# Performance work log

Hardware: AMD Instinct MI355X
Metric: run time of the kernel (lower is better)

Reference implementation:

```python
import jax, jax.numpy as jnp
import numpy as np

NQ, NT, BSZ, E, NH = 100, 197, 128, 768, 12
HD = E // NH
EPS = 1e-12  # torch F.normalize default eps


def _l2norm(x, axis=-1):
    n = jnp.linalg.norm(x, axis=axis, keepdims=True)
    return x / jnp.maximum(n, EPS)


def setup_inputs() -> dict:
    rng = jax.random.key(0)
    ks = jax.random.split(rng, 10)
    s = 0.02  # xavier-ish scale for weights
    return {
        "query": jax.random.normal(ks[0], (NQ, BSZ, E), jnp.float32),
        "key": jax.random.normal(ks[1], (NT, BSZ, E), jnp.float32),
        "value": jax.random.normal(ks[2], (NT, BSZ, E), jnp.float32),
        "in_proj_weight": jax.random.normal(ks[3], (3 * E, E), jnp.float32) * s,
        "in_proj_bias": jnp.zeros((3 * E,), jnp.float32),
        "out_proj_weight": jax.random.normal(ks[4], (E, E), jnp.float32) * s,
        "out_proj_bias": jnp.zeros((E,), jnp.float32),
        "temperature": jnp.ones((NH, 1, 1), jnp.float32),
        "q_mapper": jax.random.normal(ks[5], (1, NT, NQ), jnp.float32),
        "x_mapper": jax.random.normal(ks[6], (1, NQ, NT), jnp.float32),
    }


def reference(query, key, value, in_proj_weight, in_proj_bias,
              out_proj_weight, out_proj_bias, temperature, q_mapper, x_mapper):
    nq, bsz, e = query.shape
    nt = key.shape[0]
    # packed in-projection: split into q/k/v weights
    wq, wk, wv = jnp.split(in_proj_weight, 3, axis=0)
    bq, bk, bv = jnp.split(in_proj_bias, 3, axis=0)
    q = query @ wq.T + bq   # [Nq, bsz, E]
    k = key @ wk.T + bk     # [Nt, bsz, E]
    v = value @ wv.T + bv   # [Nt, bsz, E]
    # reshape to [bsz, nh, hd, N] (channel-major for cross-covariance attn)
    q = q.reshape(nq, bsz, NH, HD).transpose(1, 2, 3, 0)  # [b, h, d, Nq]
    k = k.reshape(nt, bsz, NH, HD).transpose(1, 2, 3, 0)  # [b, h, d, Nt]
    v = v.reshape(nt, bsz, NH, HD).transpose(1, 2, 3, 0)  # [b, h, d, Nt]
    # normalize channel vectors over tokens
    qn = _l2norm(q)
    kn = _l2norm(k)
    # mappers: normalize over last dim, then shape to [Nq, Nt] operators
    qm_op = _l2norm(q_mapper[0])  # [Nt, Nq] normalized over Nq; transpose below
    xm_op = _l2norm(x_mapper[0])  # [Nq, Nt] normalized over Nt
    # qm = q @ q_mapper^T : [b,h,d,Nq] x [Nq,Nt] -> [b,h,d,Nt]
    qm = jnp.einsum('bhdq,tq->bhdt', qn, qm_op)
    # cross-covariance attention over channels: [b,h,d,d]
    attn = jnp.einsum('bhdt,bhet->bhde', qm, kn) * temperature[None]  # temp [nh,1,1] broadcasts per-head
    attn = jax.nn.softmax(attn, axis=-1)
    x = jnp.einsum('bhde,bhet->bhdt', attn, v)        # [b,h,d,Nt]
    out = jnp.einsum('bhdt,qt->bhdq', x, xm_op)       # [b,h,d,Nq]
    # back to [Nq, bsz, E]
    out = out.transpose(3, 0, 1, 2).reshape(nq, bsz, e)
    out = out @ out_proj_weight.T + out_proj_bias
    return out
```

## Files before the change

kernel.cpp:

```cpp
#include <hip/hip_runtime.h>
#include <hip/hip_bf16.h>

using bf16 = __hip_bfloat16;

constexpr int NQ  = 100;
constexpr int NT  = 197;
constexpr int BSZ = 128;
constexpr int EMB = 768;
constexpr int NHD = 12;
constexpr int HDD = 64;
constexpr int COLS = BSZ * EMB;
constexpr int M_Q  = NQ * BSZ;
constexpr int M_KV = NT * BSZ;
constexpr int TPAD = 224;

constexpr size_t OFF_QP   = 256;
constexpr size_t SZ_QP    = (size_t)M_Q  * EMB * 4;
constexpr size_t OFF_A    = OFF_QP + SZ_QP;
constexpr size_t SZ_A     = (size_t)M_KV * EMB * 4;
constexpr size_t OFF_QINV = OFF_A + SZ_A;
constexpr size_t OFF_KINV = OFF_QINV + (size_t)COLS * 4;
constexpr size_t OFF_QMN  = OFF_KINV + (size_t)COLS * 4;
constexpr size_t OFF_XMN  = OFF_QMN + (size_t)NT * 128 * 4;
constexpr size_t OFF_G    = OFF_XMN + (size_t)NT * 128 * 4;
constexpr size_t OFF_W    = OFF_G + (size_t)COLS * 128 * 4;
constexpr size_t OFF_ZB   = OFF_QMN + 57344;
constexpr size_t OFF_G2   = OFF_G + (size_t)COLS * 128 * 2;
constexpr size_t OFF_WI16 = OFF_W + (size_t)COLS * TPAD * 2;
constexpr size_t OFF_QNT  = OFF_A + 20971520;
constexpr size_t OFF_WO16 = OFF_A + 46137344;

__device__ __forceinline__ float dl(const float* p) { return *p; }
__device__ __forceinline__ float dl(const bf16* p) { return __bfloat162float(*p); }

__device__ __forceinline__ ushort f2bf(float x) {
    union { float f; unsigned u; } v; v.f = x;
    unsigned r = v.u + 0x7FFFu + ((v.u >> 16) & 1u);
    return (ushort)(r >> 16);
}
__device__ __forceinline__ float bf2f(ushort x) {
    union { unsigned u; float f; } v; v.u = (unsigned)x << 16;
    return v.f;
}
__device__ __forceinline__ void dstore(float* p, float v) { *p = v; }
__device__ __forceinline__ void dstore(bf16* p, float v) { *p = __float2bfloat16(v); }

typedef __attribute__((ext_vector_type(8))) short short8;
typedef __attribute__((ext_vector_type(4))) short shortv4;
typedef __attribute__((ext_vector_type(4))) float f32x4;

__device__ __forceinline__ void gload16(const bf16* g, ushort* l) {
    __builtin_amdgcn_global_load_lds(
        (const __attribute__((address_space(1))) unsigned int*)g,
        (__attribute__((address_space(3))) unsigned int*)l, 16, 0, 0);
}

__device__ __forceinline__ int2 xcd_swz(int bx, int by, int gx, int gy) {
    const int nwg = gx * gy;
    const int L = by * gx + bx;
    const int q = nwg >> 3, r = nwg & 7;
    const int c = L & 7, i = L >> 3;
    const int wg = (c < r ? c * (q + 1) : r * (q + 1) + (c - r) * q) + i;
    return make_int2(wg % gx, wg / gx);
}

__global__ void k_zero(float* p, int n) {
    int i = blockIdx.x * 256 + threadIdx.x;
    if (i < n) p[i] = 0.f;
}

__global__ __launch_bounds__(256) void k_cvt(const float* __restrict__ src,
        bf16* __restrict__ dst, int n) {
    int i = (blockIdx.x * 256 + threadIdx.x) * 8;
    if (i >= n) return;
    float4 a = *(const float4*)(src + i), b = *(const float4*)(src + i + 4);
    short8 r;
    r[0] = (short)f2bf(a.x); r[1] = (short)f2bf(a.y); r[2] = (short)f2bf(a.z); r[3] = (short)f2bf(a.w);
    r[4] = (short)f2bf(b.x); r[5] = (short)f2bf(b.y); r[6] = (short)f2bf(b.z); r[7] = (short)f2bf(b.w);
    *(short8*)(dst + i) = r;
}

template <typename T>
__global__ __launch_bounds__(128) void k_qmn(const T* qm, bf16* dstT) {
    __shared__ float red[128];
    int t = blockIdx.x, q = threadIdx.x;
    float v = (q < NQ) ? dl(&qm[t * NQ + q]) : 0.f;
    red[q] = v * v;
    __syncthreads();
    for (int s = 64; s > 0; s >>= 1) { if (q < s) red[q] += red[q + s]; __syncthreads(); }
    float inv = 1.f / fmaxf(sqrtf(red[0]), 1e-12f);
    if (q < NQ) dstore(&dstT[(size_t)q * TPAD + t], v * inv);
}

template <typename T>
__global__ __launch_bounds__(256) void k_xmn(const T* xm, bf16* dstT) {
    __shared__ float red[256];
    int q = blockIdx.x, t = threadIdx.x;
    float v = (t < NT) ? dl(&xm[q * NT + t]) : 0.f;
    red[t] = v * v;
    __syncthreads();
    for (int s = 128; s > 0; s >>= 1) { if (t < s) red[t] += red[t + s]; __syncthreads(); }
    float inv = 1.f / fmaxf(sqrtf(red[0]), 1e-12f);
    if (t < NT) dstore(&dstT[(size_t)q * TPAD + t], v * inv);
}

template <int NR, int TP, int NORM>
__global__ __launch_bounds__(256) void k_trn(const bf16* __restrict__ src,
        bf16* __restrict__ dst) {
    __shared__ ushort tile[TP * 73];
    __shared__ float ssp[4][64];
    __shared__ float inv_s[64];
    const int col0 = blockIdx.x * 64;
    const int tid = threadIdx.x;
    const int c = tid & 63, tb = tid >> 6;
    float ss = 0.f;
#pragma unroll
    for (int it = 0; it < TP / 4; ++it) {
        int t = tb + it * 4;
        ushort v = 0;
        if (t < NR) v = *(const ushort*)&src[(size_t)t * COLS + col0 + c];
        tile[t * 73 + c] = v;
        if (NORM) { float f = bf2f(v); ss = fmaf(f, f, ss); }
    }
    if (NORM) {
        ssp[tb][c] = ss;
        __syncthreads();
        if (tid < 64) {
            float s = ssp[0][tid] + ssp[1][tid] + ssp[2][tid] + ssp[3][tid];
            inv_s[tid] = 1.f / fmaxf(sqrtf(s), 1e-12f);
        }
    }
    __syncthreads();
    constexpr int UPC = TP / 8;
#pragma unroll
    for (int it = 0; it < (64 * UPC) / 256; ++it) {
        int u = tid + it * 256;
        int cc = u / UPC, t0 = (u % UPC) * 8;
        float inv = NORM ? inv_s[cc] : 1.f;
        short8 s;
#pragma unroll
        for (int r = 0; r < 8; ++r) {
            ushort raw = tile[(t0 + r) * 73 + cc];
            s[r] = NORM ? (short)f2bf(bf2f(raw) * inv) : (short)raw;
        }
        *(short8*)&dst[(size_t)(col0 + cc) * TP + t0] = s;
    }
}

template <typename TC, typename TBias, bool CT = false>
__global__ __launch_bounds__(256) void k_gemm_mfma(
        const bf16* __restrict__ Ab, const bf16* __restrict__ Wb,
        TC* __restrict__ C, const TBias* __restrict__ bias,
        int M, int N, int K, int ldc) {
    __shared__ __align__(16) ushort As[128 * 32];
    __shared__ __align__(16) ushort Bs[128 * 32];
    const int t = threadIdx.x;
    const int2 bxy = xcd_swz(blockIdx.x, blockIdx.y, gridDim.x, gridDim.y);
    const int n0 = bxy.x * 128, m0 = bxy.y * 128;
    const int ln = t & 63, wv = t >> 6;
    const int ln15 = ln & 15, q8 = ln >> 4;
    const int mw = (wv & 1) * 64, nw = (wv >> 1) * 64;

    const int sr = ln >> 2, sk = (ln & 3) * 8;
    const bf16* gA = Ab + (size_t)(m0 + wv * 32 + sr) * K + sk;
    const bf16* gB = Wb + (size_t)(n0 + wv * 32 + sr) * K + sk;
    const size_t r16 = (size_t)16 * K;
    ushort* lA = &As[wv * 1024];
    ushort* lB = &Bs[wv * 1024];

    f32x4 acc[4][4] = {};
    for (int k0 = 0; k0 < K; k0 += 32) {
        gload16(gA + k0,       lA);
        gload16(gA + r16 + k0, lA + 512);
        gload16(gB + k0,       lB);
        gload16(gB + r16 + k0, lB + 512);
        __syncthreads();
        short8 a[4], b[4];
#pragma unroll
        for (int i = 0; i < 4; ++i)
            a[i] = *(const short8*)&As[(mw + i * 16 + ln15) * 32 + q8 * 8];
#pragma unroll
        for (int j = 0; j < 4; ++j)
            b[j] = *(const short8*)&Bs[(nw + j * 16 + ln15) * 32 + q8 * 8];
#pragma unroll
        for (int i = 0; i < 4; ++i)
#pragma unroll
            for (int j = 0; j < 4; ++j)
                acc[i][j] = __builtin_amdgcn_mfma_f32_16x16x32_bf16(a[i], b[j], acc[i][j], 0, 0, 0);
        __syncthreads();
    }
#pragma unroll
    for (int j = 0; j < 4; ++j) {
        const int n = n0 + nw + j * 16 + ln15;
        const float bv = dl(&bias[n]);
#pragma unroll
        for (int i = 0; i < 4; ++i) {
            const int mb = m0 + mw + i * 16 + q8 * 4;
            if constexpr (CT) {
                shortv4 s;
#pragma unroll
                for (int r = 0; r < 4; ++r) s[r] = (short)f2bf(acc[i][j][r] + bv);
                *(shortv4*)&C[(size_t)n * ldc + mb] = s;
            } else {
#pragma unroll
                for (int r = 0; r < 4; ++r)
                    dstore(&C[(size_t)(mb + r) * ldc + n], acc[i][j][r] + bv);
            }
        }
    }
}

template <typename T>
__global__ __launch_bounds__(256) void k_attn(
        const bf16* __restrict__ qnT, const bf16* __restrict__ g16,
        const bf16* __restrict__ w16T, const T* __restrict__ temp,
        bf16* __restrict__ xo) {
    const int h = blockIdx.x, b = blockIdx.y;
    const int tid = threadIdx.x;
    const int ln = tid & 63, wv = tid >> 6;
    const int ln15 = ln & 15, q8 = ln >> 4;
    const int colbase = b * EMB + h * HDD;
    __shared__ __align__(16) ushort smem[16384];
    char* sm = (char*)smem;

#pragma unroll
    for (int it = 0; it < 4; ++it) {
        int u = tid + it * 256;
        int e = u >> 4, q0 = (u & 15) * 8;
        short8 s = *(const short8*)&g16[(size_t)(colbase + e) * 128 + q0];
        *(short8*)(sm + ((e * 256 + q0 * 2) ^ ((e & 7) << 4))) = s;
    }
#pragma unroll
    for (int it = 0; it < 4; ++it) {
        int u = tid + it * 256;
        int d = u >> 4, q0 = (u & 15) * 8;
        short8 s = *(const short8*)&qnT[(size_t)(colbase + d) * 128 + q0];
        *(short8*)(sm + 16384 + ((d * 256 + q0 * 2) ^ ((d & 7) << 4))) = s;
    }
    __syncthreads();

    const int drow = 16 * wv + ln15;
    f32x4 acc[4] = {};
#pragma unroll
    for (int ks = 0; ks < 4; ++ks) {
        short8 bfrag = *(const short8*)(sm + 16384 +
            ((drow * 256 + ks * 64 + q8 * 16) ^ ((drow & 7) << 4)));
#pragma unroll
        for (int i = 0; i < 4; ++i) {
            int erow = i * 16 + ln15;
            short8 afrag = *(const short8*)(sm +
                ((erow * 256 + ks * 64 + q8 * 16) ^ ((erow & 7) << 4)));
            acc[i] = __builtin_amdgcn_mfma_f32_16x16x32_bf16(afrag, bfrag, acc[i], 0, 0, 0);
        }
    }

    const float tv = dl(&temp[h]);
    float p[4][4];
    float mx = -1e30f;
#pragma unroll
    for (int i = 0; i < 4; ++i)
#pragma unroll
        for (int r = 0; r < 4; ++r) { p[i][r] = acc[i][r] * tv; mx = fmaxf(mx, p[i][r]); }
    mx = fmaxf(mx, __shfl_xor(mx, 16, 64));
    mx = fmaxf(mx, __shfl_xor(mx, 32, 64));
    float sum = 0.f;
#pragma unroll
    for (int i = 0; i < 4; ++i)
#pragma unroll
        for (int r = 0; r < 4; ++r) { p[i][r] = __expf(p[i][r] - mx); sum += p[i][r]; }
    sum += __shfl_xor(sum, 16, 64);
    sum += __shfl_xor(sum, 32, 64);
    const float rs = 1.f / sum;

    __syncthreads();

#pragma unroll
    for (int i = 0; i < 4; ++i) {
        shortv4 s4;
#pragma unroll
        for (int r = 0; r < 4; ++r) s4[r] = (short)f2bf(p[i][r] * rs);
        *(shortv4*)(sm + 16384 + drow * 144 + q8 * 8 + 32 * i) = s4;
    }
#pragma unroll
    for (int it = 0; it < 4; ++it) {
        int u = tid + it * 256;
        int q = u >> 3, e0 = (u & 7) * 8;
        short8 s = *(const short8*)&w16T[(size_t)q * COLS + colbase + e0];
        *(short8*)(sm + ((q * 128 + e0 * 2) ^ ((q & 7) << 4))) = s;
    }
    __syncthreads();

    f32x4 o[7] = {};
#pragma unroll
    for (int ks = 0; ks < 2; ++ks) {
        short8 afrag = *(const short8*)(sm + 16384 + drow * 144 + ks * 64 + q8 * 16);
#pragma unroll
        for (int j = 0; j < 7; ++j) {
            int qrow = j * 16 + ln15;
            short8 bfrag = *(const short8*)(sm +
                ((qrow * 128 + ks * 64 + q8 * 16) ^ ((qrow & 7) << 4)));
            o[j] = __builtin_amdgcn_mfma_f32_16x16x32_bf16(afrag, bfrag, o[j], 0, 0, 0);
        }
    }
    const int dbase = h * HDD + 16 * wv + q8 * 4;
#pragma unroll
    for (int j = 0; j < 7; ++j) {
        int q = j * 16 + ln15;
        if (q < NQ) {
            shortv4 s4;
#pragma unroll
            for (int r = 0; r < 4; ++r) s4[r] = (short)f2bf(o[j][r]);
            *(shortv4*)&xo[(size_t)(q * BSZ + b) * EMB + dbase] = s4;
        }
    }
}

extern "C" void kernel_launch(void* const* d_in, const int* in_sizes, int n_in,
                              void* d_out, int out_size, void* d_ws, size_t ws_size,
                              hipStream_t stream) {
    char* ws = (char*)d_ws;
    bf16*   qp16  = (bf16*)(ws + OFF_QP);
    bf16*   ab16  = (bf16*)(ws + OFF_A);
    bf16*   qmnT  = (bf16*)(ws + OFF_QMN);
    bf16*   xmnT  = (bf16*)(ws + OFF_XMN);
    float*  zbias = (float*)(ws + OFF_ZB);
    bf16*   g16   = (bf16*)(ws + OFF_G);
    bf16*   w16T  = (bf16*)(ws + OFF_G2);
    bf16*   kvb   = (bf16*)(ws + OFF_W);
    bf16*   wi16  = (bf16*)(ws + OFF_WI16);
    bf16*   qb16  = (bf16*)(ws + OFF_A);
    bf16*   xo16  = (bf16*)(ws + OFF_A);
    bf16*   qnT   = (bf16*)(ws + OFF_QNT);
    bf16*   wo16  = (bf16*)(ws + OFF_WO16);

    const bool isbf = (in_sizes[0] == 19660800);

    k_zero<<<197, 256, 0, stream>>>((float*)(ws + OFF_QMN), 50432);

    if (isbf) {
        const bf16* inq = (const bf16*)d_in[0];
        const bf16* ink = (const bf16*)d_in[1];
        const bf16* inv = (const bf16*)d_in[2];
        const bf16* ipw = (const bf16*)d_in[3];
        const bf16* ipb = (const bf16*)d_in[4];

        k_qmn<bf16><<<197, 128, 0, stream>>>((const bf16*)d_in[8], qmnT);
        k_xmn<bf16><<<100, 256, 0, stream>>>((const bf16*)d_in[9], xmnT);

        k_gemm_mfma<bf16, bf16><<<dim3(6, 100), 256, 0, stream>>>(
            inq, ipw, qp16, ipb, M_Q, EMB, EMB, EMB);
        k_gemm_mfma<bf16, bf16><<<dim3(6, 197), 256, 0, stream>>>(
            ink, ipw + (size_t)EMB * EMB, ab16, ipb + EMB, M_KV, EMB, EMB, EMB);
        k_trn<NT, TPAD, 1><<<COLS / 64, 256, 0, stream>>>(ab16, kvb);
        k_gemm_mfma<bf16, float><<<dim3(1, COLS / 128), 256, 0, stream>>>(
            kvb, qmnT, g16, zbias, COLS, 128, TPAD, 128);
        k_gemm_mfma<bf16, bf16><<<dim3(6, 197), 256, 0, stream>>>(
            inv, ipw + (size_t)2 * EMB * EMB, ab16, ipb + 2 * EMB, M_KV, EMB, EMB, EMB);
        k_trn<NT, TPAD, 0><<<COLS / 64, 256, 0, stream>>>(ab16, kvb);
        k_gemm_mfma<bf16, float, true><<<dim3(1, COLS / 128), 256, 0, stream>>>(
            kvb, xmnT, w16T, zbias, COLS, 128, TPAD, COLS);
        k_trn<NQ, 128, 1><<<COLS / 64, 256, 0, stream>>>(qp16, qnT);
        k_attn<bf16><<<dim3(NHD, BSZ), 256, 0, stream>>>(
            qnT, g16, w16T, (const bf16*)d_in[7], xo16);
        k_gemm_mfma<bf16, bf16><<<dim3(6, 100), 256, 0, stream>>>(
            xo16, (const bf16*)d_in[5], (bf16*)d_out, (const bf16*)d_in[6],
            M_Q, EMB, EMB, EMB);
    } else {
        const float* ipb = (const float*)d_in[4];

        k_qmn<float><<<197, 128, 0, stream>>>((const float*)d_in[8], qmnT);
        k_xmn<float><<<100, 256, 0, stream>>>((const float*)d_in[9], xmnT);

        k_cvt<<<864, 256, 0, stream>>>((const float*)d_in[3], wi16, 3 * EMB * EMB);
        k_cvt<<<4800, 256, 0, stream>>>((const float*)d_in[0], qb16, M_Q * EMB);

        k_gemm_mfma<bf16, float><<<dim3(6, 100), 256, 0, stream>>>(
            qb16, wi16, qp16, ipb, M_Q, EMB, EMB, EMB);

        k_cvt<<<9456, 256, 0, stream>>>((const float*)d_in[1], kvb, M_KV * EMB);
        k_gemm_mfma<bf16, float><<<dim3(6, 197), 256, 0, stream>>>(
            kvb, wi16 + (size_t)EMB * EMB, ab16, ipb + EMB, M_KV, EMB, EMB, EMB);
        k_trn<NT, TPAD, 1><<<COLS / 64, 256, 0, stream>>>(ab16, kvb);
        k_gemm_mfma<bf16, float><<<dim3(1, COLS / 128), 256, 0, stream>>>(
            kvb, qmnT, g16, zbias, COLS, 128, TPAD, 128);

        k_cvt<<<9456, 256, 0, stream>>>((const float*)d_in[2], kvb, M_KV * EMB);
        k_gemm_mfma<bf16, float><<<dim3(6, 197), 256, 0, stream>>>(
            kvb, wi16 + (size_t)2 * EMB * EMB, ab16, ipb + 2 * EMB, M_KV, EMB, EMB, EMB);
        k_trn<NT, TPAD, 0><<<COLS / 64, 256, 0, stream>>>(ab16, kvb);
        k_gemm_mfma<bf16, float, true><<<dim3(1, COLS / 128), 256, 0, stream>>>(
            kvb, xmnT, w16T, zbias, COLS, 128, TPAD, COLS);

        k_trn<NQ, 128, 1><<<COLS / 64, 256, 0, stream>>>(qp16, qnT);
        k_cvt<<<288, 256, 0, stream>>>((const float*)d_in[5], wo16, EMB * EMB);

        k_attn<float><<<dim3(NHD, BSZ), 256, 0, stream>>>(
            qnT, g16, w16T, (const float*)d_in[7], xo16);

        k_gemm_mfma<float, float><<<dim3(6, 100), 256, 0, stream>>>(
            xo16, wo16, (float*)d_out, (const float*)d_in[6], M_Q, EMB, EMB, EMB);
    }
}
```

Baseline: 483.5 us.

## Batch conversions, Q/K/V projections, transposes and mapper GEMMs into fused launches

Merges the five fp32-to-bf16 conversions into one multi-segment kernel. It also fuses the three Q/K/V projection GEMMs into a single grid, the two K/V transposes into one kernel, and the two mapper GEMMs (G and W) into one launch. The workspace is re-laid out so the intermediates get separate buffers instead of being serialized through one reused buffer. This cuts kernel launches and the tail effects of small grids and gives larger grids for better CU occupancy, at the cost of more workspace memory.

Result: no change. 477.3 us (-1.3%).

```diff
diff --git a/kernel.cpp b/kernel.cpp
--- a/kernel.cpp
+++ b/kernel.cpp
@@ -14,21 +14,27 @@
 constexpr int M_KV = NT * BSZ;
 constexpr int TPAD = 224;
 
-constexpr size_t OFF_QP   = 256;
-constexpr size_t SZ_QP    = (size_t)M_Q  * EMB * 4;
-constexpr size_t OFF_A    = OFF_QP + SZ_QP;
-constexpr size_t SZ_A     = (size_t)M_KV * EMB * 4;
-constexpr size_t OFF_QINV = OFF_A + SZ_A;
-constexpr size_t OFF_KINV = OFF_QINV + (size_t)COLS * 4;
-constexpr size_t OFF_QMN  = OFF_KINV + (size_t)COLS * 4;
-constexpr size_t OFF_XMN  = OFF_QMN + (size_t)NT * 128 * 4;
-constexpr size_t OFF_G    = OFF_XMN + (size_t)NT * 128 * 4;
-constexpr size_t OFF_W    = OFF_G + (size_t)COLS * 128 * 4;
-constexpr size_t OFF_ZB   = OFF_QMN + 57344;
-constexpr size_t OFF_G2   = OFF_G + (size_t)COLS * 128 * 2;
-constexpr size_t OFF_WI16 = OFF_W + (size_t)COLS * TPAD * 2;
-constexpr size_t OFF_QNT  = OFF_A + 20971520;
-constexpr size_t OFF_WO16 = OFF_A + 46137344;
+constexpr size_t SZ_Q16  = (size_t)M_Q  * EMB * 2;
+constexpr size_t SZ_KV16 = (size_t)M_KV * EMB * 2;
+constexpr size_t SZ_WI   = (size_t)3 * EMB * EMB * 2;
+constexpr size_t SZ_T16  = (size_t)COLS * TPAD * 2;
+constexpr size_t SZ_128  = (size_t)COLS * 128 * 2;
+constexpr size_t OFF_QB   = 256;
+constexpr size_t OFF_KB   = OFF_QB + SZ_Q16;
+constexpr size_t OFF_VB   = OFF_KB + SZ_KV16;
+constexpr size_t OFF_WI   = OFF_VB + SZ_KV16;
+constexpr size_t OFF_QP16 = OFF_WI + SZ_WI;
+constexpr size_t OFF_KP16 = OFF_QP16 + SZ_Q16;
+constexpr size_t OFF_VP16 = OFF_KP16 + SZ_KV16;
+constexpr size_t OFF_QMNT = OFF_VP16 + SZ_KV16;
+constexpr size_t OFF_XMNT = OFF_QMNT + 57344;
+constexpr size_t OFF_WO   = OFF_XMNT + 57344;
+constexpr size_t OFF_KPT  = 256;
+constexpr size_t OFF_VPT  = OFF_KPT + SZ_T16;
+constexpr size_t OFF_W16T = OFF_VPT + SZ_T16;
+constexpr size_t OFF_QNT  = OFF_KP16;
+constexpr size_t OFF_G16  = OFF_VP16;
+constexpr size_t OFF_XO   = 256;
 
 __device__ __forceinline__ float dl(const float* p) { return *p; }
 __device__ __forceinline__ float dl(const bf16* p) { return __bfloat162float(*p); }
@@ -69,15 +75,25 @@
     if (i < n) p[i] = 0.f;
 }
 
-__global__ __launch_bounds__(256) void k_cvt(const float* __restrict__ src,
-        bf16* __restrict__ dst, int n) {
-    int i = (blockIdx.x * 256 + threadIdx.x) * 8;
-    if (i >= n) return;
-    float4 a = *(const float4*)(src + i), b = *(const float4*)(src + i + 4);
+__global__ __launch_bounds__(256) void k_cvt5(
+        const float* __restrict__ s0, bf16* __restrict__ d0,
+        const float* __restrict__ s1, bf16* __restrict__ d1,
+        const float* __restrict__ s2, bf16* __restrict__ d2,
+        const float* __restrict__ s3, bf16* __restrict__ d3,
+        const float* __restrict__ s4, bf16* __restrict__ d4) {
+    int bk = blockIdx.x;
+    const float* s; bf16* d; int lb;
+    if      (bk < 864)   { s = s0; d = d0; lb = bk; }
+    else if (bk < 5664)  { s = s1; d = d1; lb = bk - 864; }
+    else if (bk < 15120) { s = s2; d = d2; lb = bk - 5664; }
+    else if (bk < 24576) { s = s3; d = d3; lb = bk - 15120; }
+    else                 { s = s4; d = d4; lb = bk - 24576; }
+    size_t i = ((size_t)lb * 256 + threadIdx.x) * 8;
+    float4 a = *(const float4*)(s + i), b = *(const float4*)(s + i + 4);
     short8 r;
     r[0] = (short)f2bf(a.x); r[1] = (short)f2bf(a.y); r[2] = (short)f2bf(a.z); r[3] = (short)f2bf(a.w);
     r[4] = (short)f2bf(b.x); r[5] = (short)f2bf(b.y); r[6] = (short)f2bf(b.z); r[7] = (short)f2bf(b.w);
-    *(short8*)(dst + i) = r;
+    *(short8*)(d + i) = r;
 }
 
 template <typename T>
@@ -147,7 +163,182 @@
     }
 }
 
-template <typename TC, typename TBias, bool CT = false>
+__global__ __launch_bounds__(256) void k_trn2(const bf16* __restrict__ kp,
+        const bf16* __restrict__ vp, bf16* __restrict__ kpT, bf16* __restrict__ vpT) {
+    __shared__ ushort tile[TPAD * 73];
+    __shared__ float ssp[4][64];
+    __shared__ float inv_s[64];
+    const int bk = blockIdx.x;
+    const bool vseg = bk >= 1536;
+    const bf16* src = vseg ? vp : kp;
+    bf16* dst = vseg ? vpT : kpT;
+    const int col0 = (vseg ? bk - 1536 : bk) * 64;
+    const int tid = threadIdx.x;
+    const int c = tid & 63, tb = tid >> 6;
+    float ss = 0.f;
+#pragma unroll
+    for (int it = 0; it < TPAD / 4; ++it) {
+        int t = tb + it * 4;
+        ushort v = 0;
+        if (t < NT) v = *(const ushort*)&src[(size_t)t * COLS + col0 + c];
+        tile[t * 73 + c] = v;
+        if (!vseg) { float f = bf2f(v); ss = fmaf(f, f, ss); }
+    }
+    if (!vseg) {
+        ssp[tb][c] = ss;
+        __syncthreads();
+        if (tid < 64) {
+            float s = ssp[0][tid] + ssp[1][tid] + ssp[2][tid] + ssp[3][tid];
+            inv_s[tid] = 1.f / fmaxf(sqrtf(s), 1e-12f);
+        }
+    }
+    __syncthreads();
+    constexpr int UPC = TPAD / 8;
+#pragma unroll
+    for (int it = 0; it < (64 * UPC) / 256; ++it) {
+        int u = tid + it * 256;
+        int cc = u / UPC, t0 = (u % UPC) * 8;
+        float inv = vseg ? 1.f : inv_s[cc];
+        short8 s;
+#pragma unroll
+        for (int r = 0; r < 8; ++r) {
+            ushort raw = tile[(t0 + r) * 73 + cc];
+            s[r] = vseg ? (short)raw : (short)f2bf(bf2f(raw) * inv);
+        }
+        *(short8*)&dst[(size_t)(col0 + cc) * TPAD + t0] = s;
+    }
+}
+
+template <typename TBias>
+__global__ __launch_bounds__(256) void k_proj(
+        const bf16* __restrict__ Aq, const bf16* __restrict__ Ak, const bf16* __restrict__ Av,
+        const bf16* __restrict__ Wi, bf16* __restrict__ Cq, bf16* __restrict__ Ck,
+        bf16* __restrict__ Cv, const TBias* __restrict__ bias) {
+    __shared__ __align__(16) ushort As[128 * 32];
+    __shared__ __align__(16) ushort Bs[128 * 32];
+    const int t = threadIdx.x;
+    const int2 bxy = xcd_swz(blockIdx.x, blockIdx.y, gridDim.x, gridDim.y);
+    int byy = bxy.y, seg, lby;
+    if (byy < 100)      { seg = 0; lby = byy; }
+    else if (byy < 297) { seg = 1; lby = byy - 100; }
+    else                { seg = 2; lby = byy - 297; }
+    const bf16* Ab = seg == 0 ? Aq : (seg == 1 ? Ak : Av);
+    const bf16* Wb = Wi + (size_t)seg * EMB * EMB;
+    bf16* C = seg == 0 ? Cq : (seg == 1 ? Ck : Cv);
+    const TBias* bp = bias + seg * EMB;
+    const int n0 = bxy.x * 128, m0 = lby * 128;
+    const int ln = t & 63, wv = t >> 6;
+    const int ln15 = ln & 15, q8 = ln >> 4;
+    const int mw = (wv & 1) * 64, nw = (wv >> 1) * 64;
+
+    const int sr = ln >> 2, sk = (ln & 3) * 8;
+    const bf16* gA = Ab + (size_t)(m0 + wv * 32 + sr) * EMB + sk;
+    const bf16* gB = Wb + (size_t)(n0 + wv * 32 + sr) * EMB + sk;
+    const size_t r16 = (size_t)16 * EMB;
+    ushort* lA = &As[wv * 1024];
+    ushort* lB = &Bs[wv * 1024];
+
+    f32x4 acc[4][4] = {};
+    for (int k0 = 0; k0 < EMB; k0 += 32) {
+        gload16(gA + k0,       lA);
+        gload16(gA + r16 + k0, lA + 512);
+        gload16(gB + k0,       lB);
+        gload16(gB + r16 + k0, lB + 512);
+        __syncthreads();
+        short8 a[4], b[4];
+#pragma unroll
+        for (int i = 0; i < 4; ++i)
+            a[i] = *(const short8*)&As[(mw + i * 16 + ln15) * 32 + q8 * 8];
+#pragma unroll
+        for (int j = 0; j < 4; ++j)
+            b[j] = *(const short8*)&Bs[(nw + j * 16 + ln15) * 32 + q8 * 8];
+#pragma unroll
+        for (int i = 0; i < 4; ++i)
+#pragma unroll
+            for (int j = 0; j < 4; ++j)
+                acc[i][j] = __builtin_amdgcn_mfma_f32_16x16x32_bf16(a[i], b[j], acc[i][j], 0, 0, 0);
+        __syncthreads();
+    }
+#pragma unroll
+    for (int j = 0; j < 4; ++j) {
+        const int n = n0 + nw + j * 16 + ln15;
+        const float bv = dl(&bp[n]);
+#pragma unroll
+        for (int i = 0; i < 4; ++i) {
+            const int mb = m0 + mw + i * 16 + q8 * 4;
+#pragma unroll
+            for (int r = 0; r < 4; ++r)
+                dstore(&C[(size_t)(mb + r) * EMB + n], acc[i][j][r] + bv);
+        }
+    }
+}
+
+__global__ __launch_bounds__(256) void k_gw(
+        const bf16* __restrict__ kpT, const bf16* __restrict__ vpT,
+        const bf16* __restrict__ qmnT, const bf16* __restrict__ xmnT,
+        bf16* __restrict__ g16, bf16* __restrict__ w16T) {
+    __shared__ __align__(16) ushort As[128 * 32];
+    __shared__ __align__(16) ushort Bs[128 * 32];
+    const int t = threadIdx.x;
+    const int2 bxy = xcd_swz(blockIdx.x, blockIdx.y, gridDim.x, gridDim.y);
+    const bool wseg = bxy.y >= 768;
+    const int lby = wseg ? bxy.y - 768 : bxy.y;
+    const bf16* Ab = wseg ? vpT : kpT;
+    const bf16* Bb = wseg ? xmnT : qmnT;
+    const int m0 = lby * 128;
+    const int ln = t & 63, wv = t >> 6;
+    const int ln15 = ln & 15, q8 = ln >> 4;
+    const int mw = (wv & 1) * 64, nw = (wv >> 1) * 64;
+
+    const int sr = ln >> 2, sk = (ln & 3) * 8;
+    const bf16* gA = Ab + (size_t)(m0 + wv * 32 + sr) * TPAD + sk;
+    const bf16* gB = Bb + (size_t)(wv * 32 + sr) * TPAD + sk;
+    const size_t r16 = (size_t)16 * TPAD;
+    ushort* lA = &As[wv * 1024];
+    ushort* lB = &Bs[wv * 1024];
+
+    f32x4 acc[4][4] = {};
+    for (int k0 = 0; k0 < TPAD; k0 += 32) {
+        gload16(gA + k0,       lA);
+        gload16(gA + r16 + k0, lA + 512);
+        gload16(gB + k0,       lB);
+        gload16(gB + r16 + k0, lB + 512);
+        __syncthreads();
+        short8 a[4], b[4];
+#pragma unroll
+        for (int i = 0; i < 4; ++i)
+            a[i] = *(const short8*)&As[(mw + i * 16 + ln15) * 32 + q8 * 8];
+#pragma unroll
+        for (int j = 0; j < 4; ++j)
+            b[j] = *(const short8*)&Bs[(nw + j * 16 + ln15) * 32 + q8 * 8];
+#pragma unroll
+        for (int i = 0; i < 4; ++i)
+#pragma unroll
+            for (int j = 0; j < 4; ++j)
+                acc[i][j] = __builtin_amdgcn_mfma_f32_16x16x32_bf16(a[i], b[j], acc[i][j], 0, 0, 0);
+        __syncthreads();
+    }
+#pragma unroll
+    for (int j = 0; j < 4; ++j) {
+        const int n = nw + j * 16 + ln15;
+#pragma unroll
+        for (int i = 0; i < 4; ++i) {
+            const int mb = m0 + mw + i * 16 + q8 * 4;
+            if (wseg) {
+                shortv4 s;
+#pragma unroll
+                for (int r = 0; r < 4; ++r) s[r] = (short)f2bf(acc[i][j][r]);
+                *(shortv4*)&w16T[(size_t)n * COLS + mb] = s;
+            } else {
+#pragma unroll
+                for (int r = 0; r < 4; ++r)
+                    dstore(&g16[(size_t)(mb + r) * 128 + n], acc[i][j][r]);
+            }
+        }
+    }
+}
+
+template <typename TC, typename TBias>
 __global__ __launch_bounds__(256) void k_gemm_mfma(
         const bf16* __restrict__ Ab, const bf16* __restrict__ Wb,
         TC* __restrict__ C, const TBias* __restrict__ bias,
@@ -196,16 +387,9 @@
 #pragma unroll
         for (int i = 0; i < 4; ++i) {
             const int mb = m0 + mw + i * 16 + q8 * 4;
-            if constexpr (CT) {
-                shortv4 s;
-#pragma unroll
-                for (int r = 0; r < 4; ++r) s[r] = (short)f2bf(acc[i][j][r] + bv);
-                *(shortv4*)&C[(size_t)n * ldc + mb] = s;
-            } else {
-#pragma unroll
-                for (int r = 0; r < 4; ++r)
-                    dstore(&C[(size_t)(mb + r) * ldc + n], acc[i][j][r] + bv);
-            }
+#pragma unroll
+            for (int r = 0; r < 4; ++r)
+                dstore(&C[(size_t)(mb + r) * ldc + n], acc[i][j][r] + bv);
         }
     }
 }
@@ -319,84 +503,57 @@
                               void* d_out, int out_size, void* d_ws, size_t ws_size,
                               hipStream_t stream) {
     char* ws = (char*)d_ws;
-    bf16*   qp16  = (bf16*)(ws + OFF_QP);
-    bf16*   ab16  = (bf16*)(ws + OFF_A);
-    bf16*   qmnT  = (bf16*)(ws + OFF_QMN);
-    bf16*   xmnT  = (bf16*)(ws + OFF_XMN);
-    float*  zbias = (float*)(ws + OFF_ZB);
-    bf16*   g16   = (bf16*)(ws + OFF_G);
-    bf16*   w16T  = (bf16*)(ws + OFF_G2);
-    bf16*   kvb   = (bf16*)(ws + OFF_W);
-    bf16*   wi16  = (bf16*)(ws + OFF_WI16);
-    bf16*   qb16  = (bf16*)(ws + OFF_A);
-    bf16*   xo16  = (bf16*)(ws + OFF_A);
-    bf16*   qnT   = (bf16*)(ws + OFF_QNT);
-    bf16*   wo16  = (bf16*)(ws + OFF_WO16);
+    bf16* qb16  = (bf16*)(ws + OFF_QB);
+    bf16* kb16  = (bf16*)(ws + OFF_KB);
+    bf16* vb16  = (bf16*)(ws + OFF_VB);
+    bf16* wi16  = (bf16*)(ws + OFF_WI);
+    bf16* qp16  = (bf16*)(ws + OFF_QP16);
+    bf16* kp16  = (bf16*)(ws + OFF_KP16);
+    bf16* vp16  = (bf16*)(ws + OFF_VP16);
+    bf16* qmnT  = (bf16*)(ws + OFF_QMNT);
+    bf16* xmnT  = (bf16*)(ws + OFF_XMNT);
+    bf16* wo16  = (bf16*)(ws + OFF_WO);
+    bf16* kpT   = (bf16*)(ws + OFF_KPT);
+    bf16* vpT   = (bf16*)(ws + OFF_VPT);
+    bf16* w16T  = (bf16*)(ws + OFF_W16T);
+    bf16* qnT   = (bf16*)(ws + OFF_QNT);
+    bf16* g16   = (bf16*)(ws + OFF_G16);
+    bf16* xo16  = (bf16*)(ws + OFF_XO);
 
     const bool isbf = (in_sizes[0] == 19660800);
 
-    k_zero<<<197, 256, 0, stream>>>((float*)(ws + OFF_QMN), 50432);
+    k_zero<<<112, 256, 0, stream>>>((float*)(ws + OFF_QMNT), 28672);
 
     if (isbf) {
-        const bf16* inq = (const bf16*)d_in[0];
-        const bf16* ink = (const bf16*)d_in[1];
-        const bf16* inv = (const bf16*)d_in[2];
-        const bf16* ipw = (const bf16*)d_in[3];
-        const bf16* ipb = (const bf16*)d_in[4];
-
         k_qmn<bf16><<<197, 128, 0, stream>>>((const bf16*)d_in[8], qmnT);
         k_xmn<bf16><<<100, 256, 0, stream>>>((const bf16*)d_in[9], xmnT);
-
-        k_gemm_mfma<bf16, bf16><<<dim3(6, 100), 256, 0, stream>>>(
-            inq, ipw, qp16, ipb, M_Q, EMB, EMB, EMB);
-        k_gemm_mfma<bf16, bf16><<<dim3(6, 197), 256, 0, stream>>>(
-            ink, ipw + (size_t)EMB * EMB, ab16, ipb + EMB, M_KV, EMB, EMB, EMB);
-        k_trn<NT, TPAD, 1><<<COLS / 64, 256, 0, stream>>>(ab16, kvb);
-        k_gemm_mfma<bf16, float><<<dim3(1, COLS / 128), 256, 0, stream>>>(
-            kvb, qmnT, g16, zbias, COLS, 128, TPAD, 128);
-        k_gemm_mfma<bf16, bf16><<<dim3(6, 197), 256, 0, stream>>>(
-            inv, ipw + (size_t)2 * EMB * EMB, ab16, ipb + 2 * EMB, M_KV, EMB, EMB, EMB);
-        k_trn<NT, TPAD, 0><<<COLS / 64, 256, 0, stream>>>(ab16, kvb);
-        k_gemm_mfma<bf16, float, true><<<dim3(1, COLS / 128), 256, 0, stream>>>(
-            kvb, xmnT, w16T, zbias, COLS, 128, TPAD, COLS);
+        k_proj<bf16><<<dim3(6, 494), 256, 0, stream>>>(
+            (const bf16*)d_in[0], (const bf16*)d_in[1], (const bf16*)d_in[2],
+            (const bf16*)d_in[3], qp16, kp16, vp16, (const bf16*)d_in[4]);
+        k_trn2<<<3072, 256, 0, stream>>>(kp16, vp16, kpT, vpT);
         k_trn<NQ, 128, 1><<<COLS / 64, 256, 0, stream>>>(qp16, qnT);
+        k_gw<<<dim3(1, 1536), 256, 0, stream>>>(kpT, vpT, qmnT, xmnT, g16, w16T);
         k_attn<bf16><<<dim3(NHD, BSZ), 256, 0, stream>>>(
             qnT, g16, w16T, (const bf16*)d_in[7], xo16);
         k_gemm_mfma<bf16, bf16><<<dim3(6, 100), 256, 0, stream>>>(
             xo16, (const bf16*)d_in[5], (bf16*)d_out, (const bf16*)d_in[6],
             M_Q, EMB, EMB, EMB);
     } else {
-        const float* ipb = (const float*)d_in[4];
-
         k_qmn<float><<<197, 128, 0, stream>>>((const float*)d_in[8], qmnT);
         k_xmn<float><<<100, 256, 0, stream>>>((const float*)d_in[9], xmnT);
-
-        k_cvt<<<864, 256, 0, stream>>>((const float*)d_in[3], wi16, 3 * EMB * EMB);
-        k_cvt<<<4800, 256, 0, stream>>>((const float*)d_in[0], qb16, M_Q * EMB);
-
-        k_gemm_mfma<bf16, float><<<dim3(6, 100), 256, 0, stream>>>(
-            qb16, wi16, qp16, ipb, M_Q, EMB, EMB, EMB);
-
-        k_cvt<<<9456, 256, 0, stream>>>((const float*)d_in[1], kvb, M_KV * EMB);
-        k_gemm_mfma<bf16, float><<<dim3(6, 197), 256, 0, stream>>>(
-            kvb, wi16 + (size_t)EMB * EMB, ab16, ipb + EMB, M_KV, EMB, EMB, EMB);
-        k_trn<NT, TPAD, 1><<<COLS / 64, 256, 0, stream>>>(ab16, kvb);
-        k_gemm_mfma<bf16, float><<<dim3(1, COLS / 128), 256, 0, stream>>>(
-            kvb, qmnT, g16, zbias, COLS, 128, TPAD, 128);
-
-        k_cvt<<<9456, 256, 0, stream>>>((const float*)d_in[2], kvb, M_KV * EMB);
-        k_gemm_mfma<bf16, float><<<dim3(6, 197), 256, 0, stream>>>(
-            kvb, wi16 + (size_t)2 * EMB * EMB, ab16, ipb + 2 * EMB, M_KV, EMB, EMB, EMB);
-        k_trn<NT, TPAD, 0><<<COLS / 64, 256, 0, stream>>>(ab16, kvb);
-        k_gemm_mfma<bf16, float, true><<<dim3(1, COLS / 128), 256, 0, stream>>>(
-            kvb, xmnT, w16T, zbias, COLS, 128, TPAD, COLS);
-
+        k_cvt5<<<24864, 256, 0, stream>>>(
+            (const float*)d_in[3], wi16,
+            (const float*)d_in[0], qb16,
+            (const float*)d_in[1], kb16,
+            (const float*)d_in[2], vb16,
+            (const float*)d_in[5], wo16);
+        k_proj<float><<<dim3(6, 494), 256, 0, stream>>>(
+            qb16, kb16, vb16, wi16, qp16, kp16, vp16, (const float*)d_in[4]);
+        k_trn2<<<3072, 256, 0, stream>>>(kp16, vp16, kpT, vpT);
         k_trn<NQ, 128, 1><<<COLS / 64, 256, 0, stream>>>(qp16, qnT);
-        k_cvt<<<288, 256, 0, stream>>>((const float*)d_in[5], wo16, EMB * EMB);
-
+        k_gw<<<dim3(1, 1536), 256, 0, stream>>>(kpT, vpT, qmnT, xmnT, g16, w16T);
         k_attn<float><<<dim3(NHD, BSZ), 256, 0, stream>>>(
             qnT, g16, w16T, (const float*)d_in[7], xo16);
-
         k_gemm_mfma<float, float><<<dim3(6, 100), 256, 0, stream>>>(
             xo16, wo16, (float*)d_out, (const float*)d_in[6], M_Q, EMB, EMB, EMB);
     }
```
